# Performance work log

Hardware: AMD Instinct MI355X
Metric: run time of the kernel (lower is better)

## Reference

```python
import jax, jax.numpy as jnp
import numpy as np
from jax import lax

H, W = 1024, 2048
WIN = (3, 3)            # eps=1.5 on the integer grid == 8-neighborhood (3x3 window)
MIN_SAMPLES = 4         # sklearn DBSCAN counts the point itself
MIN_CLUSTER = 30        # clusters smaller than this become noise
N_SLOTS = 26            # output channels
INT32_MAX = np.iinfo(np.int32).max


def setup_inputs() -> dict:
    key = jax.random.key(0)
    mask = jax.random.normal(key, (H, W), dtype=jnp.float32)
    return {"mask": mask}


def _minpool(x):
    # 3x3 min over int32 labels, SAME padding with +inf identity
    return lax.reduce_window(x, INT32_MAX, lax.min, WIN, (1, 1), 'SAME')


def _forward(mask):
    h, w = mask.shape
    hw = h * w
    BIG = jnp.int32(hw)  # sentinel label for 'not in any cluster'

    active = mask > 0.1
    # neighbor count in 3x3 (includes self) -> DBSCAN core condition
    cnt = lax.reduce_window(active.astype(jnp.int32), 0, lax.add, WIN, (1, 1), 'SAME')
    core = active & (cnt >= MIN_SAMPLES)

    idx2d = jnp.arange(hw, dtype=jnp.int32).reshape(h, w)
    L0 = jnp.where(core, idx2d, BIG)

    # connected components over core pixels: min-label hook (3x3 min-pool)
    # + pointer jumping (path compression) until fixpoint
    def body(st):
        L, _ = st
        Ln = jnp.where(core, jnp.minimum(L, _minpool(L)), BIG)
        flat = Ln.ravel()
        table = jnp.concatenate([flat, jnp.array([hw], jnp.int32)])  # BIG -> BIG
        flat = table[table[flat]]  # two pointer-jump hops
        Ln = flat.reshape(h, w)
        return Ln, jnp.all(Ln == L)

    def cond(st):
        return jnp.logical_not(st[1])

    L, _ = lax.while_loop(cond, body, (L0, jnp.array(False)))

    # border points: active non-core pixels with a core neighbor join the
    # (deterministically min-labeled) neighboring core cluster
    pooled = _minpool(L)
    final = jnp.where(core, L, jnp.where(active & (pooled < BIG), pooled, BIG))

    flatL = final.ravel()
    labeled = flatL < BIG
    ids = jnp.where(labeled, flatL, hw)  # noise -> extra bucket hw

    sizes = jax.ops.segment_sum(labeled.astype(jnp.int32), ids, num_segments=hw + 1)[:hw]
    col = jnp.broadcast_to(jnp.arange(w, dtype=jnp.float32), (h, w)).ravel()
    colsum = jax.ops.segment_sum(jnp.where(labeled, col, 0.0), ids, num_segments=hw + 1)[:hw]

    valid = sizes >= MIN_CLUSTER  # size filter (loc.sum() < 30 -> noise)
    means = jnp.where(valid, colsum / jnp.maximum(sizes, 1), jnp.inf)
    order = jnp.argsort(means)  # valid clusters first, sorted by mean column
    rank = jnp.zeros(hw, jnp.int32).at[order].set(jnp.arange(hw, dtype=jnp.int32))

    lab = jnp.where(labeled, flatL, 0)
    ch = rank[lab]
    pix_ok = labeled & valid[lab] & (ch < N_SLOTS)
    ch2d = jnp.where(pix_ok, ch, N_SLOTS).reshape(h, w)  # N_SLOTS == 'no channel'
    # scatter 1s into the rank-th channel
    return (ch2d[None] == jnp.arange(N_SLOTS, dtype=jnp.int32)[:, None, None]).astype(jnp.uint8)


def reference(mask):
    return _forward(mask)
```

## Files before the change

### kernel.cpp

```cpp
#include <hip/hip_runtime.h>
#include <stdint.h>

#define HH 1024
#define WW 2048
#define HWN (HH*WW)
#define BIGL HWN
#define NSLOTS 26
#define MINCL 30
#define THREADS 256
#define MAXCAND 70000
#define HSZ 512
#define TILE 4096
#define NTILES 512

__device__ __forceinline__ int uf_load(int* p, int i) {
    return __hip_atomic_load(&p[i], __ATOMIC_RELAXED, __HIP_MEMORY_SCOPE_AGENT);
}
__device__ __forceinline__ void uf_store(int* p, int i, int v) {
    __hip_atomic_store(&p[i], v, __ATOMIC_RELAXED, __HIP_MEMORY_SCOPE_AGENT);
}
__device__ int uf_find(int* parent, int x) {
    int p = uf_load(parent, x);
    while (p != x) {
        int gp = uf_load(parent, p);
        if (gp != p) uf_store(parent, x, gp);
        x = p; p = gp;
    }
    return p;
}
__device__ void uf_union(int* parent, int a, int b) {
    int ra = uf_find(parent, a);
    int rb = uf_find(parent, b);
    while (ra != rb) {
        if (ra > rb) { int t = ra; ra = rb; rb = t; }
        int old = atomicCAS(&parent[rb], rb, ra);
        if (old == rb) return;
        rb = uf_find(parent, old);
        ra = uf_find(parent, ra);
    }
}

__device__ __forceinline__ int l_load(int* p, int i) {
    return __hip_atomic_load(&p[i], __ATOMIC_RELAXED, __HIP_MEMORY_SCOPE_WORKGROUP);
}
__device__ __forceinline__ void l_store(int* p, int i, int v) {
    __hip_atomic_store(&p[i], v, __ATOMIC_RELAXED, __HIP_MEMORY_SCOPE_WORKGROUP);
}
__device__ int l_find(int* lp, int x) {
    int p = l_load(lp, x);
    while (p != x) {
        int gp = l_load(lp, p);
        if (gp != p) l_store(lp, x, gp);
        x = p; p = gp;
    }
    return p;
}
__device__ void l_union(int* lp, int a, int b) {
    int ra = l_find(lp, a);
    int rb = l_find(lp, b);
    while (ra != rb) {
        if (ra > rb) { int t = ra; ra = rb; rb = t; }
        int old = atomicCAS(&lp[rb], rb, ra);
        if (old == rb) return;
        rb = l_find(lp, old);
        ra = l_find(lp, ra);
    }
}

__global__ __launch_bounds__(THREADS) void k_local(const float* __restrict__ mask,
                                                   uint8_t* __restrict__ flags,
                                                   int* __restrict__ parent) {
    __shared__ uint8_t lact[66 * 72];
    __shared__ uint8_t lc8[TILE];
    __shared__ int lp[TILE];
    int tile_x = blockIdx.x & 31, tile_y = blockIdx.x >> 5;
    int r0 = tile_y << 6, c0 = tile_x << 6;
    int tx = threadIdx.x & 15, ty = threadIdx.x >> 4;
    for (int yy = ty; yy < 66; yy += 16) {
        int gr = r0 - 1 + yy;
        for (int xx = tx; xx < 66; xx += 16) {
            int gc = c0 - 1 + xx;
            bool a = false;
            if ((unsigned)gr < HH && (unsigned)gc < WW)
                a = mask[gr * WW + gc] > 0.1f;
            lact[yy * 72 + xx] = a ? 1 : 0;
        }
    }
    __syncthreads();
    for (int li = threadIdx.x; li < TILE; li += THREADS) {
        int lr = li >> 6, lc = li & 63;
        int b = (lr + 1) * 72 + (lc + 1);
        int a = lact[b];
        int cnt = lact[b - 73] + lact[b - 72] + lact[b - 71]
                + lact[b - 1]  + a           + lact[b + 1]
                + lact[b + 71] + lact[b + 72] + lact[b + 73];
        lc8[li] = (uint8_t)(a | ((a && cnt >= 4) ? 2 : 0));
        lp[li] = li;
    }
    __syncthreads();
    {
        int row = threadIdx.x >> 2, chunk = threadIdx.x & 3;
        ((uint4*)(flags + (size_t)(r0 + row) * WW + c0))[chunk] =
            ((const uint4*)lc8)[row * 4 + chunk];
    }
    for (int li = threadIdx.x; li < TILE; li += THREADS) {
        if (!(lc8[li] & 2)) continue;
        int lr = li >> 6, lc = li & 63;
        if (lc > 0 && (lc8[li - 1] & 2)) l_union(lp, li, li - 1);
        if (lr > 0) {
            if (lc > 0  && (lc8[li - 65] & 2)) l_union(lp, li, li - 65);
            if (           (lc8[li - 64] & 2)) l_union(lp, li, li - 64);
            if (lc < 63 && (lc8[li - 63] & 2)) l_union(lp, li, li - 63);
        }
    }
    __syncthreads();
    for (int li = threadIdx.x; li < TILE; li += THREADS) {
        if (!(lc8[li] & 2)) continue;
        int root = li, p;
        while ((p = lp[root]) != root) root = p;
        int gi = (r0 + (li >> 6)) * WW + c0 + (li & 63);
        int gr = (r0 + (root >> 6)) * WW + c0 + (root & 63);
        parent[gi] = gr;
    }
}

__global__ __launch_bounds__(THREADS) void k_merge(const uint8_t* __restrict__ flags,
                                                   int* __restrict__ parent) {
    int tile_x = blockIdx.x & 31, tile_y = blockIdx.x >> 5;
    int r0 = tile_y << 6, c0 = tile_x << 6;
    int t = threadIdx.x;
    int lane = t & 63;

    if (t < 64) {
        int r = r0, c = c0 + t, i = r * WW + c;
        bool selfC = (flags[i] & 2) != 0;
        bool nC = false, nwC = false, neC = false;
        if (selfC && r > 0) {
            nC  = (flags[i - WW] & 2) != 0;
            nwC = (c > 0)      && (flags[i - WW - 1] & 2);
            neC = (c < WW - 1) && (flags[i - WW + 1] & 2);
        }
        int did = 0, ra = -1, rb = -1;
        if (selfC && r > 0 && nC) { ra = uf_find(parent, i); rb = uf_find(parent, i - WW); did = 1; }
        int pra = __shfl_up(ra, 1), prb = __shfl_up(rb, 1), pdid = __shfl_up(did, 1);
        bool head = (lane == 0) || !pdid || pra != ra || prb != rb;
        if (did && head) uf_union(parent, ra, rb);
        if (selfC && r > 0) {
            if (t == 0) {
                if (nwC) uf_union(parent, i, i - WW - 1);
                if (!nC && neC) uf_union(parent, i, i - WW + 1);
            } else if (t == 63) {
                if (!nC && nwC) uf_union(parent, i, i - WW - 1);
                if (neC) {
                    bool eC = (c < WW - 1) && (flags[i + 1] & 2);
                    if (!eC) uf_union(parent, i, i - WW + 1);
                }
            } else if (!nC) {
                if (nwC) uf_union(parent, i, i - WW - 1);
                if (neC) uf_union(parent, i, i - WW + 1);
            }
        }
        if (t == 0 && selfC && c > 0 && (flags[i - 1] & 2))
            uf_union(parent, i, i - 1);
    } else if (t < 127) {
        int lr = t - 63;
        int r = r0 + lr, c = c0, i = r * WW + c;
        bool selfC = (flags[i] & 2) != 0;
        bool wC = false, nwC = false;
        if (selfC && c > 0) {
            wC  = (flags[i - 1] & 2) != 0;
            nwC = (flags[i - WW - 1] & 2) != 0;
        }
        int did = 0, ra = -1, rb = -1;
        if (selfC && wC) { ra = uf_find(parent, i); rb = uf_find(parent, i - 1); did = 1; }
        int pra = __shfl_up(ra, 1), prb = __shfl_up(rb, 1), pdid = __shfl_up(did, 1);
        bool head = (lane == 0) || !pdid || pra != ra || prb != rb;
        if (did && head) uf_union(parent, ra, rb);
        if (selfC && !wC && nwC) uf_union(parent, i, i - WW - 1);
    } else if (t < 190) {
        int lr = t - 126;
        int r = r0 + lr, c = c0 + 63, i = r * WW + c;
        bool selfC = (flags[i] & 2) != 0;
        if (selfC && c < WW - 1) {
            bool neC = (flags[i - WW + 1] & 2) != 0;
            bool eC  = (flags[i + 1] & 2) != 0;
            if (neC && !eC) uf_union(parent, i, i - WW + 1);
        }
    }
}

__global__ __launch_bounds__(THREADS) void k_border_stats(
        const uint8_t* __restrict__ flags, int* __restrict__ parent,
        int* __restrict__ labfull, int* __restrict__ sizes,
        unsigned long long* __restrict__ colsum) {
    __shared__ int h_lab[HSZ];
    __shared__ int h_sz[HSZ];
    __shared__ unsigned long long h_cs[HSZ];
    for (int t = threadIdx.x; t < HSZ; t += THREADS) {
        h_lab[t] = -1; h_sz[t] = 0; h_cs[t] = 0;
    }
    __syncthreads();

    int i = blockIdx.x * THREADS + threadIdx.x;
    int f = flags[i];
    int lab = BIGL;
    if (f & 2) {
        lab = uf_find(parent, i);
    } else if (f & 1) {
        int r = i >> 11, c = i & (WW - 1);
        int m = BIGL;
        #pragma unroll
        for (int dr = -1; dr <= 1; ++dr) {
            int rr = r + dr;
            if (rr < 0 || rr >= HH) continue;
            #pragma unroll
            for (int dc = -1; dc <= 1; ++dc) {
                int cc = c + dc;
                if (cc < 0 || cc >= WW) continue;
                int n = rr * WW + cc;
                if (flags[n] & 2) {
                    int v = uf_find(parent, n);
                    if (v < m) m = v;
                }
            }
        }
        lab = m;
    }
    labfull[i] = lab;

    int lane = threadIdx.x & 63;
    int labp = __shfl_up(lab, 1);
    bool head = (lane == 0) || (labp != lab);
    unsigned long long hm = __ballot(head);
    if (head && lab < BIGL) {
        unsigned long long rest = (hm >> lane) >> 1;
        int len = rest ? __ffsll((unsigned long long)rest) : (64 - lane);
        long long c0 = (long long)(i & (WW - 1));
        unsigned long long csum =
            (unsigned long long)(c0 * len + (long long)len * (len - 1) / 2);
        unsigned slot = (((unsigned)lab * 2654435761u) >> 20) & (HSZ - 1);
        for (;;) {
            int old = atomicCAS(&h_lab[slot], -1, lab);
            if (old == -1 || old == lab) {
                atomicAdd(&h_sz[slot], len);
                atomicAdd(&h_cs[slot], csum);
                break;
            }
            slot = (slot + 1) & (HSZ - 1);
        }
    }
    __syncthreads();
    for (int t = threadIdx.x; t < HSZ; t += THREADS) {
        int lb = h_lab[t];
        if (lb >= 0) {
            atomicAdd(&sizes[lb], h_sz[t]);
            atomicAdd(&colsum[lb], h_cs[t]);
        }
    }
}

__global__ __launch_bounds__(THREADS) void k_cands(const int* __restrict__ sizes,
                                                   const unsigned long long* __restrict__ colsum,
                                                   unsigned long long* __restrict__ cand,
                                                   int* __restrict__ counter) {
    int i = blockIdx.x * THREADS + threadIdx.x;
    int s = sizes[i];
    if (s >= MINCL) {
        float mean = (float)colsum[i] / (float)s;
        unsigned int mb = __float_as_uint(mean);
        unsigned long long key = ((unsigned long long)mb << 32) | (unsigned int)i;
        int p = atomicAdd(counter, 1);
        cand[p] = key;
    }
}

__global__ __launch_bounds__(1024) void k_select(const unsigned long long* __restrict__ cand,
                                                 const int* __restrict__ counter,
                                                 signed char* __restrict__ chan) {
    __shared__ unsigned long long sm[1024];
    const int tid = threadIdx.x;
    const int n = *counter;
    unsigned long long prev = 0;
    for (int k = 0; k < NSLOTS; ++k) {
        unsigned long long local = ~0ull;
        for (int j = tid; j < n; j += 1024) {
            unsigned long long v = cand[j];
            if ((k == 0 || v > prev) && v < local) local = v;
        }
        sm[tid] = local;
        __syncthreads();
        for (int s = 512; s > 0; s >>= 1) {
            if (tid < s && sm[tid + s] < sm[tid]) sm[tid] = sm[tid + s];
            __syncthreads();
        }
        unsigned long long best = sm[0];
        __syncthreads();
        if (best == ~0ull) break;
        if (tid == 0) chan[(unsigned int)(best & 0xFFFFFFFFull)] = (signed char)k;
        prev = best;
    }
}

__global__ __launch_bounds__(THREADS) void k_output(const int* __restrict__ labfull,
                                                    const signed char* __restrict__ chan,
                                                    int* __restrict__ out) {
    int i4 = (blockIdx.x * THREADS + threadIdx.x) * 4;
    int chv[4];
    #pragma unroll
    for (int t = 0; t < 4; ++t) {
        int lab = labfull[i4 + t];
        chv[t] = (lab < BIGL) ? (int)chan[lab] : -1;
    }
    #pragma unroll
    for (int c = 0; c < NSLOTS; ++c) {
        int4 v;
        v.x = (chv[0] == c) ? 1 : 0;
        v.y = (chv[1] == c) ? 1 : 0;
        v.z = (chv[2] == c) ? 1 : 0;
        v.w = (chv[3] == c) ? 1 : 0;
        *(int4*)(out + (size_t)c * HWN + i4) = v;
    }
}

extern "C" void kernel_launch(void* const* d_in, const int* in_sizes, int n_in,
                              void* d_out, int out_size, void* d_ws, size_t ws_size,
                              hipStream_t stream) {
    const float* mask = (const float*)d_in[0];
    int* out = (int*)d_out;

    char* w = (char*)d_ws;
    int* parent                 = (int*)(w);
    int* labfull                = (int*)(w + (size_t)HWN * 4);
    int* sizes                  = (int*)(w + (size_t)HWN * 8);
    unsigned long long* colsum  = (unsigned long long*)(w + (size_t)HWN * 12);
    uint8_t* flags              = (uint8_t*)(w + (size_t)HWN * 20);
    signed char* chan           = (signed char*)(w + (size_t)HWN * 21);
    unsigned long long* cand    = (unsigned long long*)(w + (size_t)HWN * 22);
    int* counter                = (int*)(w + (size_t)HWN * 22 + MAXCAND * 8);

    hipMemsetAsync(sizes, 0, (size_t)HWN * 4, stream);
    hipMemsetAsync(colsum, 0, (size_t)HWN * 8, stream);
    hipMemsetAsync(chan, 0xFF, (size_t)HWN, stream);
    hipMemsetAsync(counter, 0, 4, stream);

    const int blocks = HWN / THREADS;
    k_local       <<<NTILES, THREADS, 0, stream>>>(mask, flags, parent);
    k_merge       <<<NTILES, THREADS, 0, stream>>>(flags, parent);
    k_border_stats<<<blocks, THREADS, 0, stream>>>(flags, parent, labfull, sizes, colsum);
    k_cands       <<<blocks, THREADS, 0, stream>>>(sizes, colsum, cand, counter);
    k_select      <<<1, 1024, 0, stream>>>(cand, counter, chan);
    k_output      <<<HWN / (4 * THREADS), THREADS, 0, stream>>>(labfull, chan, out);
}
```

Measured before the change: 423.3 us.

## Flatten labels once, fuse candidate gathering into stats, prune local unions

Result: slower. 454.4 us (+7.3%).

```diff
diff --git a/kernel.cpp b/kernel.cpp
--- a/kernel.cpp
+++ b/kernel.cpp
@@ -106,11 +106,17 @@
     for (int li = threadIdx.x; li < TILE; li += THREADS) {
         if (!(lc8[li] & 2)) continue;
         int lr = li >> 6, lc = li & 63;
-        if (lc > 0 && (lc8[li - 1] & 2)) l_union(lp, li, li - 1);
+        bool w = (lc > 0) && (lc8[li - 1] & 2);
+        if (w) l_union(lp, li, li - 1);
         if (lr > 0) {
-            if (lc > 0  && (lc8[li - 65] & 2)) l_union(lp, li, li - 65);
-            if (           (lc8[li - 64] & 2)) l_union(lp, li, li - 64);
-            if (lc < 63 && (lc8[li - 63] & 2)) l_union(lp, li, li - 63);
+            bool n = (lc8[li - 64] & 2) != 0;
+            if (n) {
+                l_union(lp, li, li - 64);
+            } else {
+                if (!w && lc > 0 && (lc8[li - 65] & 2)) l_union(lp, li, li - 65);
+                if (lc < 63 && !(lc8[li + 1] & 2) && (lc8[li - 63] & 2))
+                    l_union(lp, li, li - 63);
+            }
         }
     }
     __syncthreads();
@@ -189,10 +195,24 @@
     }
 }
 
+__global__ __launch_bounds__(THREADS) void k_flatten(const uint8_t* __restrict__ flags,
+                                                     int* __restrict__ parent,
+                                                     int* __restrict__ finalL) {
+    int i4 = (blockIdx.x * THREADS + threadIdx.x) * 4;
+    uchar4 f = *(const uchar4*)(flags + i4);
+    int4 o;
+    o.x = (f.x & 2) ? uf_find(parent, i4)     : BIGL;
+    o.y = (f.y & 2) ? uf_find(parent, i4 + 1) : BIGL;
+    o.z = (f.z & 2) ? uf_find(parent, i4 + 2) : BIGL;
+    o.w = (f.w & 2) ? uf_find(parent, i4 + 3) : BIGL;
+    *(int4*)(finalL + i4) = o;
+}
+
 __global__ __launch_bounds__(THREADS) void k_border_stats(
-        const uint8_t* __restrict__ flags, int* __restrict__ parent,
+        const uint8_t* __restrict__ flags, const int* __restrict__ finalL,
         int* __restrict__ labfull, int* __restrict__ sizes,
-        unsigned long long* __restrict__ colsum) {
+        unsigned long long* __restrict__ colsum,
+        int* __restrict__ cand, int* __restrict__ counter) {
     __shared__ int h_lab[HSZ];
     __shared__ int h_sz[HSZ];
     __shared__ unsigned long long h_cs[HSZ];
@@ -205,7 +225,7 @@
     int f = flags[i];
     int lab = BIGL;
     if (f & 2) {
-        lab = uf_find(parent, i);
+        lab = finalL[i];
     } else if (f & 1) {
         int r = i >> 11, c = i & (WW - 1);
         int m = BIGL;
@@ -217,11 +237,8 @@
             for (int dc = -1; dc <= 1; ++dc) {
                 int cc = c + dc;
                 if (cc < 0 || cc >= WW) continue;
-                int n = rr * WW + cc;
-                if (flags[n] & 2) {
-                    int v = uf_find(parent, n);
-                    if (v < m) m = v;
-                }
+                int v = finalL[rr * WW + cc];
+                if (v < m) m = v;
             }
         }
         lab = m;
@@ -253,29 +270,21 @@
     for (int t = threadIdx.x; t < HSZ; t += THREADS) {
         int lb = h_lab[t];
         if (lb >= 0) {
-            atomicAdd(&sizes[lb], h_sz[t]);
+            int add = h_sz[t];
+            int old = atomicAdd(&sizes[lb], add);
+            if (old < MINCL && old + add >= MINCL) {
+                int p = atomicAdd(counter, 1);
+                cand[p] = lb;
+            }
             atomicAdd(&colsum[lb], h_cs[t]);
         }
     }
 }
 
-__global__ __launch_bounds__(THREADS) void k_cands(const int* __restrict__ sizes,
-                                                   const unsigned long long* __restrict__ colsum,
-                                                   unsigned long long* __restrict__ cand,
-                                                   int* __restrict__ counter) {
-    int i = blockIdx.x * THREADS + threadIdx.x;
-    int s = sizes[i];
-    if (s >= MINCL) {
-        float mean = (float)colsum[i] / (float)s;
-        unsigned int mb = __float_as_uint(mean);
-        unsigned long long key = ((unsigned long long)mb << 32) | (unsigned int)i;
-        int p = atomicAdd(counter, 1);
-        cand[p] = key;
-    }
-}
-
-__global__ __launch_bounds__(1024) void k_select(const unsigned long long* __restrict__ cand,
+__global__ __launch_bounds__(1024) void k_select(const int* __restrict__ cand,
                                                  const int* __restrict__ counter,
+                                                 const int* __restrict__ sizes,
+                                                 const unsigned long long* __restrict__ colsum,
                                                  signed char* __restrict__ chan) {
     __shared__ unsigned long long sm[1024];
     const int tid = threadIdx.x;
@@ -284,7 +293,10 @@
     for (int k = 0; k < NSLOTS; ++k) {
         unsigned long long local = ~0ull;
         for (int j = tid; j < n; j += 1024) {
-            unsigned long long v = cand[j];
+            int lab = cand[j];
+            float mean = (float)colsum[lab] / (float)sizes[lab];
+            unsigned long long v =
+                ((unsigned long long)__float_as_uint(mean) << 32) | (unsigned int)lab;
             if ((k == 0 || v > prev) && v < local) local = v;
         }
         sm[tid] = local;
@@ -330,13 +342,14 @@
 
     char* w = (char*)d_ws;
     int* parent                 = (int*)(w);
-    int* labfull                = (int*)(w + (size_t)HWN * 4);
+    int* finalL                 = (int*)(w + (size_t)HWN * 4);
     int* sizes                  = (int*)(w + (size_t)HWN * 8);
     unsigned long long* colsum  = (unsigned long long*)(w + (size_t)HWN * 12);
     uint8_t* flags              = (uint8_t*)(w + (size_t)HWN * 20);
     signed char* chan           = (signed char*)(w + (size_t)HWN * 21);
-    unsigned long long* cand    = (unsigned long long*)(w + (size_t)HWN * 22);
-    int* counter                = (int*)(w + (size_t)HWN * 22 + MAXCAND * 8);
+    int* labfull                = (int*)(w + (size_t)HWN * 22);
+    int* cand                   = (int*)(w + (size_t)HWN * 26);
+    int* counter                = (int*)(w + (size_t)HWN * 26 + MAXCAND * 4);
 
     hipMemsetAsync(sizes, 0, (size_t)HWN * 4, stream);
     hipMemsetAsync(colsum, 0, (size_t)HWN * 8, stream);
@@ -346,8 +359,9 @@
     const int blocks = HWN / THREADS;
     k_local       <<<NTILES, THREADS, 0, stream>>>(mask, flags, parent);
     k_merge       <<<NTILES, THREADS, 0, stream>>>(flags, parent);
-    k_border_stats<<<blocks, THREADS, 0, stream>>>(flags, parent, labfull, sizes, colsum);
-    k_cands       <<<blocks, THREADS, 0, stream>>>(sizes, colsum, cand, counter);
-    k_select      <<<1, 1024, 0, stream>>>(cand, counter, chan);
+    k_flatten     <<<HWN / (4 * THREADS), THREADS, 0, stream>>>(flags, parent, finalL);
+    k_border_stats<<<blocks, THREADS, 0, stream>>>(flags, finalL, labfull, sizes, colsum,
+                                                   cand, counter);
+    k_select      <<<1, 1024, 0, stream>>>(cand, counter, sizes, colsum, chan);
     k_output      <<<HWN / (4 * THREADS), THREADS, 0, stream>>>(labfull, chan, out);
 }
```

## Emit size-threshold candidates in stats kernel and rank-select top slots in one block

Applied to the files above, without the earlier changes.

New measurement: 1.185 ms. +180.1%, slower.

```diff
diff --git a/kernel.cpp b/kernel.cpp
--- a/kernel.cpp
+++ b/kernel.cpp
@@ -12,6 +12,7 @@
 #define HSZ 512
 #define TILE 4096
 #define NTILES 512
+#define SELN 8192
 
 __device__ __forceinline__ int uf_load(int* p, int i) {
     return __hip_atomic_load(&p[i], __ATOMIC_RELAXED, __HIP_MEMORY_SCOPE_AGENT);
@@ -192,7 +193,8 @@
 __global__ __launch_bounds__(THREADS) void k_border_stats(
         const uint8_t* __restrict__ flags, int* __restrict__ parent,
         int* __restrict__ labfull, int* __restrict__ sizes,
-        unsigned long long* __restrict__ colsum) {
+        unsigned long long* __restrict__ colsum,
+        int* __restrict__ cand, int* __restrict__ counter) {
     __shared__ int h_lab[HSZ];
     __shared__ int h_sz[HSZ];
     __shared__ unsigned long long h_cs[HSZ];
@@ -253,51 +255,50 @@
     for (int t = threadIdx.x; t < HSZ; t += THREADS) {
         int lb = h_lab[t];
         if (lb >= 0) {
-            atomicAdd(&sizes[lb], h_sz[t]);
+            int add = h_sz[t];
+            int old = atomicAdd(&sizes[lb], add);
+            if (old < MINCL && old + add >= MINCL) {
+                int p = atomicAdd(counter, 1);
+                cand[p] = lb;
+            }
             atomicAdd(&colsum[lb], h_cs[t]);
         }
     }
 }
 
-__global__ __launch_bounds__(THREADS) void k_cands(const int* __restrict__ sizes,
-                                                   const unsigned long long* __restrict__ colsum,
-                                                   unsigned long long* __restrict__ cand,
-                                                   int* __restrict__ counter) {
-    int i = blockIdx.x * THREADS + threadIdx.x;
-    int s = sizes[i];
-    if (s >= MINCL) {
-        float mean = (float)colsum[i] / (float)s;
-        unsigned int mb = __float_as_uint(mean);
-        unsigned long long key = ((unsigned long long)mb << 32) | (unsigned int)i;
-        int p = atomicAdd(counter, 1);
-        cand[p] = key;
-    }
-}
-
-__global__ __launch_bounds__(1024) void k_select(const unsigned long long* __restrict__ cand,
-                                                 const int* __restrict__ counter,
-                                                 signed char* __restrict__ chan) {
-    __shared__ unsigned long long sm[1024];
+__global__ __launch_bounds__(THREADS) void k_select(const int* __restrict__ cand,
+                                                    const int* __restrict__ counter,
+                                                    const int* __restrict__ sizes,
+                                                    const unsigned long long* __restrict__ colsum,
+                                                    signed char* __restrict__ chan) {
+    __shared__ unsigned long long keys[SELN];
     const int tid = threadIdx.x;
     const int n = *counter;
-    unsigned long long prev = 0;
-    for (int k = 0; k < NSLOTS; ++k) {
-        unsigned long long local = ~0ull;
-        for (int j = tid; j < n; j += 1024) {
-            unsigned long long v = cand[j];
-            if ((k == 0 || v > prev) && v < local) local = v;
-        }
-        sm[tid] = local;
-        __syncthreads();
-        for (int s = 512; s > 0; s >>= 1) {
-            if (tid < s && sm[tid + s] < sm[tid]) sm[tid] = sm[tid + s];
-            __syncthreads();
-        }
-        unsigned long long best = sm[0];
-        __syncthreads();
-        if (best == ~0ull) break;
-        if (tid == 0) chan[(unsigned int)(best & 0xFFFFFFFFull)] = (signed char)k;
-        prev = best;
+    const int nl = n < SELN ? n : SELN;
+    for (int j = tid; j < nl; j += THREADS) {
+        int lab = cand[j];
+        float mean = (float)colsum[lab] / (float)sizes[lab];
+        keys[j] = ((unsigned long long)__float_as_uint(mean) << 32) | (unsigned int)lab;
+    }
+    __syncthreads();
+    for (int i = tid; i < n; i += THREADS) {
+        unsigned long long ki;
+        if (i < SELN) ki = keys[i];
+        else {
+            int lab = cand[i];
+            float mean = (float)colsum[lab] / (float)sizes[lab];
+            ki = ((unsigned long long)__float_as_uint(mean) << 32) | (unsigned int)lab;
+        }
+        int rank = 0;
+        for (int j = 0; j < nl && rank < NSLOTS; ++j) rank += (keys[j] < ki) ? 1 : 0;
+        for (int j = SELN; j < n && rank < NSLOTS; ++j) {
+            int lab = cand[j];
+            float mean = (float)colsum[lab] / (float)sizes[lab];
+            unsigned long long kj =
+                ((unsigned long long)__float_as_uint(mean) << 32) | (unsigned int)lab;
+            rank += (kj < ki) ? 1 : 0;
+        }
+        if (rank < NSLOTS) chan[(unsigned int)(ki & 0xFFFFFFFFull)] = (signed char)rank;
     }
 }
 
@@ -335,8 +336,8 @@
     unsigned long long* colsum  = (unsigned long long*)(w + (size_t)HWN * 12);
     uint8_t* flags              = (uint8_t*)(w + (size_t)HWN * 20);
     signed char* chan           = (signed char*)(w + (size_t)HWN * 21);
-    unsigned long long* cand    = (unsigned long long*)(w + (size_t)HWN * 22);
-    int* counter                = (int*)(w + (size_t)HWN * 22 + MAXCAND * 8);
+    int* cand                   = (int*)(w + (size_t)HWN * 22);
+    int* counter                = (int*)(w + (size_t)HWN * 22 + MAXCAND * 4);
 
     hipMemsetAsync(sizes, 0, (size_t)HWN * 4, stream);
     hipMemsetAsync(colsum, 0, (size_t)HWN * 8, stream);
@@ -346,8 +347,8 @@
     const int blocks = HWN / THREADS;
     k_local       <<<NTILES, THREADS, 0, stream>>>(mask, flags, parent);
     k_merge       <<<NTILES, THREADS, 0, stream>>>(flags, parent);
-    k_border_stats<<<blocks, THREADS, 0, stream>>>(flags, parent, labfull, sizes, colsum);
-    k_cands       <<<blocks, THREADS, 0, stream>>>(sizes, colsum, cand, counter);
-    k_select      <<<1, 1024, 0, stream>>>(cand, counter, chan);
+    k_border_stats<<<blocks, THREADS, 0, stream>>>(flags, parent, labfull, sizes, colsum,
+                                                   cand, counter);
+    k_select      <<<1, THREADS, 0, stream>>>(cand, counter, sizes, colsum, chan);
     k_output      <<<HWN / (4 * THREADS), THREADS, 0, stream>>>(labfull, chan, out);
 }
```
